# Kernel tuning notes

Measured on AMD Instinct MI355X. Metric: run time of the kernel, lower is better.

Reference implementation:

```python
import jax, jax.numpy as jnp
import numpy as np
from jax import lax

B, NPB = 4, 100000
N = B * NPB
C_BEV, C = 256, 64
H = W = 180
S = 10          # NUM_SWEEPS
MAXI = 64       # gt_boxes.shape[1] (max instances per sample)
NUMLOC = B * MAXI * S
NUMINST = B * MAXI
PC_MIN = -54.0
CELL = 0.075 * 8  # voxel * bev_image_stride


def setup_inputs() -> dict:
    key = jax.random.key(0)
    ks = jax.random.split(key, 20)
    pb = jnp.repeat(jnp.arange(B), NPB).astype(jnp.float32)
    xy = jax.random.uniform(ks[0], (N, 2), minval=-54.0, maxval=53.9)
    z = jax.random.uniform(ks[1], (N, 1), minval=-5.0, maxval=2.9)
    extra = jax.random.uniform(ks[2], (N, 2))
    sweep = jax.random.randint(ks[3], (N, 1), 0, S).astype(jnp.float32)
    inst = jax.random.randint(ks[4], (N, 1), 0, MAXI).astype(jnp.float32)
    points = jnp.concatenate([pb[:, None], xy, z, extra, sweep, inst, inst], axis=1)
    sc = 0.05
    return {
        'points': points,
        'spatial_features_2d': jax.random.normal(ks[5], (B, C_BEV, H, W)),
        'conv_w': jax.random.normal(ks[6], (C, C_BEV, 3, 3)) * sc,
        'bn_gamma': jnp.ones((C,)), 'bn_beta': jnp.zeros((C,)),
        'w_seg': jax.random.normal(ks[7], (C, 3)) * sc, 'b_seg': jnp.zeros((3,)),
        'w_reg': jax.random.normal(ks[8], (C, 3)) * sc, 'b_reg': jnp.zeros((3,)),
        'w_emb': jax.random.normal(ks[9], (C, 2)) * sc, 'b_emb': jnp.zeros((2,)),
        'w_shape': jax.random.normal(ks[10], (3, C)) * sc, 'b_shape': jnp.zeros((C,)),
        'w_tf': jax.random.normal(ks[11], (2 * C + 6, 7)) * sc, 'b_tf': jnp.zeros((7,)),
        'w_mos': jax.random.normal(ks[12], (C + 6, 1)) * sc, 'b_mos': jnp.zeros((1,)),
    }


def _forward(points, spatial_features_2d, conv_w, bn_gamma, bn_beta,
             w_seg, b_seg, w_reg, b_reg, w_emb, b_emb,
             w_shape, b_shape, w_tf, b_tf, w_mos, b_mos):
    # ---- shared_conv: Conv3x3 (no bias) + BatchNorm2d (training stats) + ReLU
    y = lax.conv_general_dilated(spatial_features_2d, conv_w, (1, 1), 'SAME',
                                 dimension_numbers=('NCHW', 'OIHW', 'NCHW'))
    mu = y.mean(axis=(0, 2, 3), keepdims=True)
    var = y.var(axis=(0, 2, 3), keepdims=True)
    y = (y - mu) * lax.rsqrt(var + 1e-5)
    bev = jax.nn.relu(y * bn_gamma[None, :, None, None] + bn_beta[None, :, None, None])
    bev_hwc = jnp.transpose(bev, (0, 2, 3, 1))  # [B,H,W,C]

    # ---- bilinear gather of BEV features at point locations (vectorized over batch)
    pb = points[:, 0].astype(jnp.int32)
    px = (points[:, 1] - PC_MIN) / CELL
    py = (points[:, 2] - PC_MIN) / CELL
    x0 = jnp.clip(jnp.floor(px).astype(jnp.int32), 0, W - 1)
    x1 = jnp.clip(x0 + 1, 0, W - 1)
    y0 = jnp.clip(jnp.floor(py).astype(jnp.int32), 0, H - 1)
    y1 = jnp.clip(y0 + 1, 0, H - 1)
    x0f, x1f = x0.astype(px.dtype), x1.astype(px.dtype)
    y0f, y1f = y0.astype(py.dtype), y1.astype(py.dtype)
    Ia = bev_hwc[pb, y0, x0]
    Ib = bev_hwc[pb, y1, x0]
    Ic = bev_hwc[pb, y0, x1]
    Id = bev_hwc[pb, y1, x1]
    wa = ((x1f - px) * (y1f - py))[:, None]
    wb = ((x1f - px) * (py - y0f))[:, None]
    wc = ((px - x0f) * (y1f - py))[:, None]
    wd = ((px - x0f) * (py - y0f))[:, None]
    points_feat = Ia * wa + Ib * wb + Ic * wc + Id * wd  # [N, C]

    # ---- point heads (single Linear each, mid_c=None)
    points_cls_logit = points_feat @ w_seg + b_seg
    points_offset = points_feat @ w_reg + b_reg
    points_embedding = points_feat @ w_emb + b_emb

    # ---- instance / local aggregation (training branch; all points foreground)
    sweep = points[:, 6].astype(jnp.int32)
    inst = points[:, 7].astype(jnp.int32)
    seg = (pb * MAXI + inst) * S + sweep  # dense local id in [0, NUMLOC)
    cnt = jax.ops.segment_sum(jnp.ones((N,), points.dtype), seg, NUMLOC)
    nonempty = cnt > 0
    xyz = points[:, 1:4]
    centroid = jax.ops.segment_sum(xyz, seg, NUMLOC) / jnp.clip(cnt, 1.0)[:, None]
    centered = xyz - centroid[seg]

    shape_enc = jax.ops.segment_max(centered @ w_shape + b_shape, seg, NUMLOC)
    shape_enc = jnp.where(nonempty[:, None], shape_enc, 0.0)
    locals_feat = jax.ops.segment_max(points_feat, seg, NUMLOC)
    locals_feat = jnp.where(nonempty[:, None], locals_feat, 0.0)
    locals_feat = locals_feat + shape_enc  # [NUMLOC, C]

    inst_of_local = jnp.arange(NUMLOC, dtype=jnp.int32) // S
    sweep_of_local = jnp.arange(NUMLOC, dtype=jnp.int32) % S
    neg_inf = jnp.array(-jnp.inf, locals_feat.dtype)
    globals_feat = jax.ops.segment_max(
        jnp.where(nonempty[:, None], locals_feat, neg_inf), inst_of_local, NUMINST)
    inst_nonempty = jax.ops.segment_max(nonempty, inst_of_local, NUMINST)
    globals_feat = jnp.where(inst_nonempty[:, None], globals_feat, 0.0)

    max_sweep = jax.ops.segment_max(jnp.where(nonempty, sweep_of_local, -1), inst_of_local, NUMINST)
    min_sweep = jax.ops.segment_min(jnp.where(nonempty, sweep_of_local, S), inst_of_local, NUMINST)
    inst_ids = jnp.arange(NUMINST, dtype=jnp.int32)
    idx_max = jnp.clip(inst_ids * S + max_sweep, 0, NUMLOC - 1)
    idx_min = jnp.clip(inst_ids * S + min_sweep, 0, NUMLOC - 1)
    init_center = centroid[idx_min]    # [NUMINST, 3]
    target_center = centroid[idx_max]  # [NUMINST, 3]

    locals_cat = jnp.concatenate(
        [locals_feat, globals_feat[inst_of_local], centroid, target_center[inst_of_local]], axis=1)
    locals_tf = locals_cat @ w_tf + b_tf  # [NUMLOC, 7]
    inst_feat = jnp.concatenate([globals_feat, init_center, target_center], axis=1)
    inst_mos = inst_feat @ w_mos + b_mos  # [NUMINST, 1]

    return points_cls_logit, points_offset, points_embedding, locals_tf, inst_mos


def reference(points, spatial_features_2d, conv_w, bn_gamma, bn_beta,
              w_seg, b_seg, w_reg, b_reg, w_emb, b_emb,
              w_shape, b_shape, w_tf, b_tf, w_mos, b_mos):
    return _forward(points, spatial_features_2d, conv_w, bn_gamma, bn_beta,
                    w_seg, b_seg, w_reg, b_reg, w_emb, b_emb,
                    w_shape, b_shape, w_tf, b_tf, w_mos, b_mos)
```

## Files before the change

### kernel.cpp

```cpp
#include <hip/hip_runtime.h>

typedef __attribute__((ext_vector_type(8))) unsigned short u16x8;
typedef __attribute__((ext_vector_type(8))) short s16x8;
typedef __attribute__((ext_vector_type(4))) float f32x4;

#define NPTS 400000
#define HW 32400
#define WID 180
#define NCI 256
#define NCO 64
#define NSEG 2560
#define NINST 256
#define NBLK 128
#define PPB 3125

__device__ __forceinline__ float bf2f(unsigned short u) {
  union { unsigned int i; float f; } v; v.i = ((unsigned int)u) << 16; return v.f;
}
__device__ __forceinline__ unsigned short f2bf(float f) {
  unsigned int u = __float_as_uint(f);
  return (unsigned short)((u + 0x7fffu + ((u >> 16) & 1u)) >> 16);
}

__device__ __forceinline__ void gld_lds16(const void* g, void* l) {
  __builtin_amdgcn_global_load_lds((const __attribute__((address_space(1))) void*)g,
                                   (__attribute__((address_space(3))) void*)l, 16, 0, 0);
}

__global__ __launch_bounds__(256) void k_transpose(const float* __restrict__ x,
                                                   unsigned short* __restrict__ xt) {
  const int bw = blockIdx.x;
  const int h = blockIdx.y, b = blockIdx.z;
  const int w0 = (bw >> 2) * 64, ci0 = (bw & 3) * 64;
  __shared__ float tile[64][68];
  const int t = threadIdx.x;
  const int a = t & 15, c4 = t >> 4;
  const int w4 = a * 4;
  const bool ldok = (w0 + w4) < WID;
#pragma unroll
  for (int it = 0; it < 4; ++it) {
    int ci = c4 + it * 16;
    float4 v = make_float4(0.f, 0.f, 0.f, 0.f);
    if (ldok) v = *(const float4*)(x + ((size_t)(b * NCI + ci0 + ci) * WID + h) * WID + w0 + w4);
    tile[w4 + 0][ci] = v.x;
    tile[w4 + 1][ci] = v.y;
    tile[w4 + 2][ci] = v.z;
    tile[w4 + 3][ci] = v.w;
  }
  __syncthreads();
  const int q = t & 7, r = t >> 3;
#pragma unroll
  for (int it = 0; it < 2; ++it) {
    int wl = r + it * 32;
    int w = w0 + wl;
    if (w >= WID) continue;
    const float* row = &tile[wl][q * 8];
    float4 lo = *(const float4*)(row);
    float4 hi = *(const float4*)(row + 4);
    u16x8 o;
    o[0] = f2bf(lo.x); o[1] = f2bf(lo.y); o[2] = f2bf(lo.z); o[3] = f2bf(lo.w);
    o[4] = f2bf(hi.x); o[5] = f2bf(hi.y); o[6] = f2bf(hi.z); o[7] = f2bf(hi.w);
    *(u16x8*)(xt + ((size_t)((b * WID + h) * WID + w)) * NCI + ci0 + q * 8) = o;
  }
}

__global__ void k_wreorg(const float* __restrict__ wt, unsigned short* __restrict__ wb) {
  int id = blockIdx.x * 256 + threadIdx.x;
  if (id >= 9 * 8 * 64 * 32) return;
  int cw = id & 31;
  int co = (id >> 5) & 63;
  int chunk = (id >> 11) & 7;
  int tap = id >> 14;
  int ci = chunk * 32 + cw;
  wb[id] = f2bf(wt[((size_t)co * 256 + ci) * 9 + tap]);
}

#define ROWB 6272
#define RBUF 25600
__global__ __launch_bounds__(256, 3) void k_conv_mfma(const unsigned short* __restrict__ xt,
                                                   const unsigned short* __restrict__ wb,
                                                   const float* __restrict__ zbuf,
                                                   unsigned short* __restrict__ y) {
  const int wg = blockIdx.x;
  const int lin = (wg & 7) * 90 + (wg >> 3);
  const int h2 = lin % 90;
  const int t2 = lin / 90;
  const int wth = t2 & 1, b = t2 >> 1;
  const int h0 = h2 * 2;
  const int w0 = wth * 96;
  __shared__ unsigned char strip[2][RBUF];
  const int tid = threadIdx.x;
  const int lane = tid & 63, wv = tid >> 6;
  const int mh = wv >> 1, nh = wv & 1;
  const int l15 = lane & 15, lk = lane >> 4;

  const char* srcs[7];
#pragma unroll
  for (int k = 0; k < 7; ++k) {
    int j = wv + k * 4;
    int g = j * 64 + lane;
    int pxlin = g >> 2, sub = g & 3;
    int row = pxlin / 98;
    int px = pxlin - row * 98;
    int hh = h0 + row - 1;
    int worig = w0 + px - 1;
    bool valid = (j < 25) && (pxlin < 392) &&
                 (hh >= 0) && (hh < WID) && (worig >= 0) && (worig < WID);
    int cig = sub ^ ((px >> 1) & 3);
    srcs[k] = valid
        ? (const char*)(xt + ((size_t)((b * WID + hh) * WID + worig)) * NCI + cig * 8)
        : (const char*)zbuf + lane * 16;
  }

  f32x4 acc[6][2];
#pragma unroll
  for (int i = 0; i < 6; ++i)
#pragma unroll
    for (int j = 0; j < 2; ++j) { acc[i][j][0] = 0.f; acc[i][j][1] = 0.f; acc[i][j][2] = 0.f; acc[i][j][3] = 0.f; }

  auto stage = [&](unsigned char* buf, int chunk) {
#pragma unroll
    for (int k = 0; k < 7; ++k) {
      int j = wv + k * 4;
      if (j >= 25) break;
      gld_lds16(srcs[k] + chunk * 64, buf + j * 1024);
    }
  };

  stage(strip[0], 0);
  asm volatile("s_waitcnt vmcnt(0)" ::: "memory");
  __syncthreads();

  const unsigned short* wco[2];
#pragma unroll
  for (int nf = 0; nf < 2; ++nf)
    wco[nf] = wb + (size_t)((nh * 2 + nf) * 16 + l15) * 32 + lk * 8;

  for (int chunk = 0; chunk < 8; ++chunk) {
    s16x8 bfr[9][2];
#pragma unroll
    for (int tap = 0; tap < 9; ++tap)
#pragma unroll
      for (int nf = 0; nf < 2; ++nf)
        bfr[tap][nf] = *(const s16x8*)(wco[nf] + (size_t)(tap * 8 + chunk) * 2048);
    if (chunk < 7) stage(strip[(chunk + 1) & 1], chunk + 1);
    const unsigned char* buf = strip[chunk & 1];
#pragma unroll
    for (int tap = 0; tap < 9; ++tap) {
      const int dh = tap / 3, dw = tap % 3;
      s16x8 afr[6];
#pragma unroll
      for (int i = 0; i < 6; ++i) {
        int wp = i * 16 + l15 + dw;
        int byte = (mh + dh) * ROWB + wp * 64 + ((lk ^ ((wp >> 1) & 3)) * 16);
        afr[i] = *(const s16x8*)(buf + byte);
      }
#pragma unroll
      for (int i = 0; i < 6; ++i)
#pragma unroll
        for (int nf = 0; nf < 2; ++nf)
          acc[i][nf] = __builtin_amdgcn_mfma_f32_16x16x32_bf16(afr[i], bfr[tap][nf], acc[i][nf], 0, 0, 0);
    }
    asm volatile("s_waitcnt vmcnt(0)" ::: "memory");
    __syncthreads();
  }

  const int r4 = lk * 4;
  const int hrow = h0 + mh;
#pragma unroll
  for (int i = 0; i < 6; ++i) {
#pragma unroll
    for (int nf = 0; nf < 2; ++nf) {
      int co = (nh * 2 + nf) * 16 + l15;
#pragma unroll
      for (int j = 0; j < 4; ++j) {
        int w = w0 + i * 16 + r4 + j;
        if (w < WID)
          y[((size_t)(b * HW) + hrow * WID + w) * 64 + co] = f2bf(acc[i][nf][j]);
      }
    }
  }
}

__global__ void k_stats2(const unsigned short* __restrict__ y, float* __restrict__ part) {
  const int t = threadIdx.x;
  const int c2 = (t & 31) * 2;
  const int g = t >> 5;
  float s0 = 0.f, s1 = 0.f, ss0 = 0.f, ss1 = 0.f;
  for (int r = blockIdx.x * 8 + g; r < 4 * HW; r += 256 * 8) {
    unsigned int v = *(const unsigned int*)(y + (size_t)r * 64 + c2);
    float f0 = bf2f((unsigned short)(v & 0xffffu));
    float f1 = bf2f((unsigned short)(v >> 16));
    s0 += f0; ss0 = fmaf(f0, f0, ss0);
    s1 += f1; ss1 = fmaf(f1, f1, ss1);
  }
  __shared__ float ls[8][64], lss[8][64];
  ls[g][c2] = s0; ls[g][c2 + 1] = s1;
  lss[g][c2] = ss0; lss[g][c2 + 1] = ss1;
  __syncthreads();
  if (t < 64) {
    float s = 0.f, ss = 0.f;
    for (int k = 0; k < 8; ++k) { s += ls[k][t]; ss += lss[k][t]; }
    part[(blockIdx.x * 64 + t) * 2] = s;
    part[(blockIdx.x * 64 + t) * 2 + 1] = ss;
  }
}

__global__ void k_bnparams(const float* __restrict__ part, const float* __restrict__ gamma,
                           const float* __restrict__ beta, float* __restrict__ ab) {
  const int t = threadIdx.x;
  float s = 0.f, ss = 0.f;
  for (int k = 0; k < 256; ++k) { s += part[(k * 64 + t) * 2]; ss += part[(k * 64 + t) * 2 + 1]; }
  float mu = s / 129600.f;
  float var = ss / 129600.f - mu * mu;
  float a = rsqrtf(var + 1e-5f) * gamma[t];
  ab[t * 2] = a; ab[t * 2 + 1] = beta[t] - mu * a;
}

__global__ void k_bn2(const unsigned short* __restrict__ y, const float* __restrict__ ab,
                      unsigned short* __restrict__ bev) {
  __shared__ float sa[64], sb[64];
  const int t = threadIdx.x;
  if (t < 64) { sa[t] = ab[t * 2]; sb[t] = ab[t * 2 + 1]; }
  __syncthreads();
  size_t id = (size_t)blockIdx.x * 256 + t;
  if (id >= (size_t)4 * HW * 8) return;
  int c0 = (int)(id & 7) * 8;
  u16x8 v = *(const u16x8*)(y + id * 8);
  u16x8 o;
#pragma unroll
  for (int k = 0; k < 8; ++k) {
    float f = fmaf(bf2f(v[k]), sa[c0 + k], sb[c0 + k]);
    o[k] = f2bf(f > 0.f ? f : 0.f);
  }
  *(u16x8*)(bev + id * 8) = o;
}

__global__ __launch_bounds__(256) void k_points(const float* __restrict__ pts,
                         const unsigned short* __restrict__ bev,
                         unsigned short* __restrict__ pf) {
  const int gid = blockIdx.x * 256 + threadIdx.x;
  const int lane = gid & 63;
  const int wid = gid >> 6;
#pragma unroll
  for (int it = 0; it < 4; ++it) {
    int p = wid * 4 + it;
    const float* pr = pts + (size_t)p * 9;
    float pbf = pr[0], xx = pr[1], yy = pr[2];
    int b = (int)pbf;
    float px = (xx - (-54.0f)) / 0.6f;
    float py = (yy - (-54.0f)) / 0.6f;
    int x0 = (int)floorf(px); x0 = min(max(x0, 0), WID - 1);
    int x1 = min(x0 + 1, WID - 1);
    int y0 = (int)floorf(py); y0 = min(max(y0, 0), WID - 1);
    int y1 = min(y0 + 1, WID - 1);
    float x0f = (float)x0, x1f = (float)x1, y0f = (float)y0, y1f = (float)y1;
    float wa = (x1f - px) * (y1f - py);
    float wb = (x1f - px) * (py - y0f);
    float wc = (px - x0f) * (y1f - py);
    float wd = (px - x0f) * (py - y0f);
    int i00 = y0 * WID + x0;
    int dx = x1 - x0;
    int dy = (y1 - y0) * WID;
    const unsigned short* bb = bev + ((size_t)b * HW) * 64 + lane;
    float Ia = bf2f(bb[(size_t)i00 * 64]);
    float Ic = bf2f(bb[(size_t)(i00 + dx) * 64]);
    float Ib = bf2f(bb[(size_t)(i00 + dy) * 64]);
    float Id = bf2f(bb[(size_t)(i00 + dy + dx) * 64]);
    float f = wa * Ia + wb * Ib + wc * Ic + wd * Id;
    pf[(size_t)p * 64 + lane] = f2bf(f);
  }
}

__global__ void k_heads(const unsigned short* __restrict__ pf,
                        const float* __restrict__ wseg, const float* __restrict__ bseg,
                        const float* __restrict__ wreg, const float* __restrict__ breg,
                        const float* __restrict__ wemb, const float* __restrict__ bemb,
                        float* __restrict__ ocls, float* __restrict__ ooff, float* __restrict__ oemb) {
  const int p = blockIdx.x * 256 + threadIdx.x;
  if (p >= NPTS) return;
  float a0 = bseg[0], a1 = bseg[1], a2 = bseg[2];
  float r0 = breg[0], r1 = breg[1], r2 = breg[2];
  float e0 = bemb[0], e1 = bemb[1];
  const u16x8* q = (const u16x8*)(pf + (size_t)p * 64);
#pragma unroll
  for (int g = 0; g < 8; ++g) {
    u16x8 v8 = q[g];
#pragma unroll
    for (int k = 0; k < 8; ++k) {
      int kk = g * 8 + k;
      float v = bf2f(v8[k]);
      a0 = fmaf(v, wseg[kk * 3 + 0], a0);
      a1 = fmaf(v, wseg[kk * 3 + 1], a1);
      a2 = fmaf(v, wseg[kk * 3 + 2], a2);
      r0 = fmaf(v, wreg[kk * 3 + 0], r0);
      r1 = fmaf(v, wreg[kk * 3 + 1], r1);
      r2 = fmaf(v, wreg[kk * 3 + 2], r2);
      e0 = fmaf(v, wemb[kk * 2 + 0], e0);
      e1 = fmaf(v, wemb[kk * 2 + 1], e1);
    }
  }
  ocls[p * 3 + 0] = a0; ocls[p * 3 + 1] = a1; ocls[p * 3 + 2] = a2;
  ooff[p * 3 + 0] = r0; ooff[p * 3 + 1] = r1; ooff[p * 3 + 2] = r2;
  oemb[p * 2 + 0] = e0; oemb[p * 2 + 1] = e1;
}

__global__ __launch_bounds__(256) void k_hist2(const float* __restrict__ pts,
                                               int* __restrict__ seg, int* __restrict__ rankp,
                                               int* __restrict__ bh) {
  __shared__ int lc[NSEG];
  const int t = threadIdx.x, blk = blockIdx.x;
  for (int i = t; i < NSEG; i += 256) lc[i] = 0;
  __syncthreads();
  const int p0 = blk * PPB;
  for (int i = t; i < PPB; i += 256) {
    int p = p0 + i;
    const float* pr = pts + (size_t)p * 9;
    int b = (int)pr[0];
    int sw = (int)pr[6];
    int ins = (int)pr[7];
    int s = (b * 64 + ins) * 10 + sw;
    seg[p] = s;
    rankp[p] = atomicAdd(&lc[s], 1);
  }
  __syncthreads();
  for (int i = t; i < NSEG; i += 256) bh[i * NBLK + blk] = lc[i];
}

__global__ void k_scan2a(const int* __restrict__ bh, int* __restrict__ basebk,
                         int* __restrict__ tot) {
  const int s = blockIdx.x * 256 + threadIdx.x;
  int acc = 0;
  for (int b = 0; b < NBLK; ++b) {
    int v = bh[s * NBLK + b];
    basebk[s * NBLK + b] = acc;
    acc += v;
  }
  tot[s] = acc;
}

__global__ void k_scan2b(const int* __restrict__ tot, int* __restrict__ base,
                         int* __restrict__ cnt) {
  __shared__ int csum[256];
  const int t = threadIdx.x;
  int loc[10]; int run = 0;
#pragma unroll
  for (int k = 0; k < 10; ++k) { loc[k] = tot[t * 10 + k]; run += loc[k]; }
  csum[t] = run;
  __syncthreads();
  if (t == 0) {
    int a = 0;
    for (int i = 0; i < 256; ++i) { int v = csum[i]; csum[i] = a; a += v; }
  }
  __syncthreads();
  int acc = csum[t];
#pragma unroll
  for (int k = 0; k < 10; ++k) {
    int s = t * 10 + k;
    base[s] = acc; cnt[s] = loc[k];
    acc += loc[k];
  }
}

__global__ void k_scatter2(const int* __restrict__ seg, const int* __restrict__ rankp,
                           const int* __restrict__ base, const int* __restrict__ basebk,
                           int* __restrict__ order) {
  const int p = blockIdx.x * 256 + threadIdx.x;
  if (p < NPTS) {
    int s = seg[p];
    int blk = p / PPB;
    order[base[s] + basebk[s * NBLK + blk] + rankp[p]] = p;
  }
}

__global__ __launch_bounds__(256) void k_seg(const int* __restrict__ cnt, const int* __restrict__ base,
                      const int* __restrict__ order, const float* __restrict__ pts,
                      const unsigned short* __restrict__ pf,
                      const float* __restrict__ wsh, const float* __restrict__ bsh,
                      float* __restrict__ lf, float* __restrict__ centroid,
                      int* __restrict__ nonempty) {
  const int s = blockIdx.x;
  const int t = threadIdx.x, lane = t & 63, wv = t >> 6;
  const int n = cnt[s], bs = base[s];
  float sx = 0.f, sy = 0.f, sz = 0.f;
  for (int i = t; i < n; i += 256) {
    int p = order[bs + i];
    const float* pr = pts + (size_t)p * 9;
    sx += pr[1]; sy += pr[2]; sz += pr[3];
  }
#pragma unroll
  for (int m = 32; m > 0; m >>= 1) {
    sx += __shfl_xor(sx, m); sy += __shfl_xor(sy, m); sz += __shfl_xor(sz, m);
  }
  __shared__ float red[3][4];
  __shared__ float csh[3];
  if (lane == 0) { red[0][wv] = sx; red[1][wv] = sy; red[2][wv] = sz; }
  __syncthreads();
  if (t == 0) {
    float dn = (float)max(n, 1);
    csh[0] = (red[0][0] + red[0][1] + red[0][2] + red[0][3]) / dn;
    csh[1] = (red[1][0] + red[1][1] + red[1][2] + red[1][3]) / dn;
    csh[2] = (red[2][0] + red[2][1] + red[2][2] + red[2][3]) / dn;
  }
  __syncthreads();
  const float cx = csh[0], cy = csh[1], cz = csh[2];
  const float w0 = wsh[lane], w1 = wsh[64 + lane], w2 = wsh[128 + lane], bb = bsh[lane];
  float smax = -INFINITY, lmax = -INFINITY;
  for (int i = wv; i < n; i += 4) {
    int p = order[bs + i];
    const float* pr = pts + (size_t)p * 9;
    float sv = fmaf(pr[1] - cx, w0, fmaf(pr[2] - cy, w1, fmaf(pr[3] - cz, w2, bb)));
    smax = fmaxf(smax, sv);
    lmax = fmaxf(lmax, bf2f(pf[(size_t)p * 64 + lane]));
  }
  __shared__ float rs[4][64], rl[4][64];
  rs[wv][lane] = smax; rl[wv][lane] = lmax;
  __syncthreads();
  if (wv == 0) {
    smax = fmaxf(fmaxf(rs[0][lane], rs[1][lane]), fmaxf(rs[2][lane], rs[3][lane]));
    lmax = fmaxf(fmaxf(rl[0][lane], rl[1][lane]), fmaxf(rl[2][lane], rl[3][lane]));
    bool ne = n > 0;
    lf[s * 64 + lane] = (ne ? lmax : 0.f) + (ne ? smax : 0.f);
    if (lane == 0) {
      nonempty[s] = ne ? 1 : 0;
      centroid[s * 3 + 0] = cx; centroid[s * 3 + 1] = cy; centroid[s * 3 + 2] = cz;
    }
  }
}

__global__ void k_glob(const float* __restrict__ lf, const int* __restrict__ ne,
                       const float* __restrict__ centroid,
                       const float* __restrict__ wmos, const float* __restrict__ bmos,
                       float* __restrict__ gf, float* __restrict__ tc, float* __restrict__ ic,
                       float* __restrict__ omos) {
  const int i = blockIdx.x;
  const int t = threadIdx.x;
  float g = -INFINITY;
  int maxsw = -1, minsw = 10;
  bool any = false;
#pragma unroll
  for (int s = 0; s < 10; ++s) {
    int idx = i * 10 + s;
    bool e = ne[idx] != 0;
    float v = lf[idx * 64 + t];
    g = fmaxf(g, e ? v : -INFINITY);
    if (e) { any = true; maxsw = s; minsw = min(minsw, s); }
  }
  float gv = any ? g : 0.f;
  gf[i * 64 + t] = gv;
  int idxmax = min(max(i * 10 + maxsw, 0), NSEG - 1);
  int idxmin = min(max(i * 10 + minsw, 0), NSEG - 1);
  float tcx = centroid[idxmax * 3 + 0], tcy = centroid[idxmax * 3 + 1], tcz = centroid[idxmax * 3 + 2];
  float icx = centroid[idxmin * 3 + 0], icy = centroid[idxmin * 3 + 1], icz = centroid[idxmin * 3 + 2];
  if (t == 0) {
    tc[i * 3 + 0] = tcx; tc[i * 3 + 1] = tcy; tc[i * 3 + 2] = tcz;
    ic[i * 3 + 0] = icx; ic[i * 3 + 1] = icy; ic[i * 3 + 2] = icz;
  }
  float r = gv * wmos[t];
#pragma unroll
  for (int m = 32; m > 0; m >>= 1) r += __shfl_xor(r, m);
  if (t == 0) {
    r += icx * wmos[64] + icy * wmos[65] + icz * wmos[66];
    r += tcx * wmos[67] + tcy * wmos[68] + tcz * wmos[69];
    omos[i] = r + bmos[0];
  }
}

__global__ void k_tf(const float* __restrict__ lf, const float* __restrict__ gf,
                     const float* __restrict__ centroid, const float* __restrict__ tc,
                     const float* __restrict__ wtf, const float* __restrict__ btf,
                     float* __restrict__ otf) {
  const int r = blockIdx.x * 256 + threadIdx.x;
  if (r >= NSEG) return;
  const int i = r / 10;
  float acc[7];
#pragma unroll
  for (int j = 0; j < 7; ++j) acc[j] = btf[j];
  for (int k = 0; k < 64; ++k) {
    float v = lf[r * 64 + k];
#pragma unroll
    for (int j = 0; j < 7; ++j) acc[j] = fmaf(v, wtf[k * 7 + j], acc[j]);
  }
  for (int k = 0; k < 64; ++k) {
    float v = gf[i * 64 + k];
#pragma unroll
    for (int j = 0; j < 7; ++j) acc[j] = fmaf(v, wtf[(64 + k) * 7 + j], acc[j]);
  }
#pragma unroll
  for (int c = 0; c < 3; ++c) {
    float v = centroid[r * 3 + c];
#pragma unroll
    for (int j = 0; j < 7; ++j) acc[j] = fmaf(v, wtf[(128 + c) * 7 + j], acc[j]);
  }
#pragma unroll
  for (int c = 0; c < 3; ++c) {
    float v = tc[i * 3 + c];
#pragma unroll
    for (int j = 0; j < 7; ++j) acc[j] = fmaf(v, wtf[(131 + c) * 7 + j], acc[j]);
  }
#pragma unroll
  for (int j = 0; j < 7; ++j) otf[r * 7 + j] = acc[j];
}

extern "C" void kernel_launch(void* const* d_in, const int* in_sizes, int n_in,
                              void* d_out, int out_size, void* d_ws, size_t ws_size,
                              hipStream_t stream) {
  const float* pts   = (const float*)d_in[0];
  const float* x     = (const float*)d_in[1];
  const float* convw = (const float*)d_in[2];
  const float* gamma = (const float*)d_in[3];
  const float* beta  = (const float*)d_in[4];
  const float* wseg  = (const float*)d_in[5];
  const float* bseg  = (const float*)d_in[6];
  const float* wreg  = (const float*)d_in[7];
  const float* breg  = (const float*)d_in[8];
  const float* wemb  = (const float*)d_in[9];
  const float* bemb  = (const float*)d_in[10];
  const float* wsh   = (const float*)d_in[11];
  const float* bsh   = (const float*)d_in[12];
  const float* wtf   = (const float*)d_in[13];
  const float* btf   = (const float*)d_in[14];
  const float* wmos  = (const float*)d_in[15];
  const float* bmos  = (const float*)d_in[16];

  float* out = (float*)d_out;
  float* o_cls = out;
  float* o_off = out + 1200000;
  float* o_emb = out + 2400000;
  float* o_tf  = out + 3200000;
  float* o_mos = out + 3217920;

  char* wsp = (char*)d_ws;
  size_t off = 0;
  auto alloc = [&](size_t bytes) -> void* {
    void* p = wsp + off;
    off = (off + bytes + 255) & ~(size_t)255;
    return p;
  };
  unsigned short* xt   = (unsigned short*)alloc((size_t)4 * WID * WID * NCI * 2);
  unsigned short* pf   = xt;
  unsigned short* wbuf = (unsigned short*)alloc((size_t)9 * 8 * 64 * 32 * 2);
  unsigned short* y    = (unsigned short*)alloc((size_t)4 * HW * 64 * 2);
  unsigned short* bev  = (unsigned short*)alloc((size_t)4 * HW * 64 * 2);
  int*   seg      = (int*)alloc((size_t)NPTS * 4);
  int*   rankp    = (int*)alloc((size_t)NPTS * 4);
  int*   order    = (int*)alloc((size_t)NPTS * 4);
  int*   bh       = (int*)alloc((size_t)NSEG * NBLK * 4);
  int*   basebk   = (int*)alloc((size_t)NSEG * NBLK * 4);
  int*   tot      = (int*)alloc(NSEG * 4);
  int*   cnt      = (int*)alloc(NSEG * 4);
  int*   base     = (int*)alloc(NSEG * 4);
  float* part     = (float*)alloc(256 * 64 * 2 * 4);
  float* ab       = (float*)alloc(64 * 2 * 4);
  float* centroid = (float*)alloc(NSEG * 3 * 4);
  float* lf       = (float*)alloc(NSEG * 64 * 4);
  int*   nonem    = (int*)alloc(NSEG * 4);
  float* gf       = (float*)alloc(NINST * 64 * 4);
  float* tc       = (float*)alloc(NINST * 3 * 4);
  float* ic       = (float*)alloc(NINST * 3 * 4);
  float* zbuf     = (float*)alloc(2048);
  (void)ws_size; (void)n_in; (void)in_sizes; (void)out_size;

  hipMemsetAsync(zbuf, 0, 2048, stream);

  k_hist2<<<NBLK, 256, 0, stream>>>(pts, seg, rankp, bh);
  k_scan2a<<<10, 256, 0, stream>>>(bh, basebk, tot);
  k_scan2b<<<1, 256, 0, stream>>>(tot, base, cnt);
  k_scatter2<<<(NPTS + 255) / 256, 256, 0, stream>>>(seg, rankp, base, basebk, order);
  k_transpose<<<dim3(12, WID, 4), 256, 0, stream>>>(x, xt);
  k_wreorg<<<576, 256, 0, stream>>>(convw, wbuf);
  k_conv_mfma<<<720, 256, 0, stream>>>(xt, wbuf, zbuf, y);
  k_stats2<<<256, 256, 0, stream>>>(y, part);
  k_bnparams<<<1, 64, 0, stream>>>(part, gamma, beta, ab);
  k_bn2<<<(4 * HW * 8 + 255) / 256, 256, 0, stream>>>(y, ab, bev);
  k_points<<<25000, 256, 0, stream>>>(pts, bev, pf);
  k_heads<<<(NPTS + 255) / 256, 256, 0, stream>>>(pf, wseg, bseg, wreg, breg, wemb, bemb,
                                                  o_cls, o_off, o_emb);
  k_seg<<<NSEG, 256, 0, stream>>>(cnt, base, order, pts, pf, wsh, bsh, lf, centroid, nonem);
  k_glob<<<NINST, 64, 0, stream>>>(lf, nonem, centroid, wmos, bmos, gf, tc, ic, o_mos);
  k_tf<<<(NSEG + 255) / 256, 256, 0, stream>>>(lf, gf, centroid, tc, wtf, btf, o_tf);
}
```

Before: 308.4 us.

## Fuse BN statistics into conv epilogue and BN-apply into point sampling

The conv kernel now accumulates per-channel sum and sum-of-squares from its fp32 accumulators and writes per-workgroup partials, so the separate stats pass over y is gone. The BN+ReLU pass that wrote a bev tensor is also removed. The affine transform and ReLU are applied on the fly to the four bilinear taps inside k_points. Separately, the histogram block count is raised and the per-segment scan is vectorised with int4. The cost is extra epilogue work and an LDS reduction in the conv, a longer serial reduction in bnparams (720 partials), and recomputing BN per sampled tap. Statistics now come from fp32 values rather than bf16-rounded ones.

```diff
diff --git a/kernel.cpp b/kernel.cpp
--- a/kernel.cpp
+++ b/kernel.cpp
@@ -11,8 +11,8 @@
 #define NCO 64
 #define NSEG 2560
 #define NINST 256
-#define NBLK 128
-#define PPB 3125
+#define NBLK 500
+#define PPB 800
 
 __device__ __forceinline__ float bf2f(unsigned short u) {
   union { unsigned int i; float f; } v; v.i = ((unsigned int)u) << 16; return v.f;
@@ -80,7 +80,8 @@
 __global__ __launch_bounds__(256, 3) void k_conv_mfma(const unsigned short* __restrict__ xt,
                                                    const unsigned short* __restrict__ wb,
                                                    const float* __restrict__ zbuf,
-                                                   unsigned short* __restrict__ y) {
+                                                   unsigned short* __restrict__ y,
+                                                   float* __restrict__ part) {
   const int wg = blockIdx.x;
   const int lin = (wg & 7) * 90 + (wg >> 3);
   const int h2 = lin % 90;
@@ -89,6 +90,7 @@
   const int h0 = h2 * 2;
   const int w0 = wth * 96;
   __shared__ unsigned char strip[2][RBUF];
+  __shared__ float redS[2][2][2][16], redQ[2][2][2][16];
   const int tid = threadIdx.x;
   const int lane = tid & 63, wv = tid >> 6;
   const int mh = wv >> 1, nh = wv & 1;
@@ -167,6 +169,7 @@
 
   const int r4 = lk * 4;
   const int hrow = h0 + mh;
+  float s[2] = {0.f, 0.f}, q[2] = {0.f, 0.f};
 #pragma unroll
   for (int i = 0; i < 6; ++i) {
 #pragma unroll
@@ -175,34 +178,29 @@
 #pragma unroll
       for (int j = 0; j < 4; ++j) {
         int w = w0 + i * 16 + r4 + j;
-        if (w < WID)
-          y[((size_t)(b * HW) + hrow * WID + w) * 64 + co] = f2bf(acc[i][nf][j]);
+        if (w < WID) {
+          float v = acc[i][nf][j];
+          y[((size_t)(b * HW) + hrow * WID + w) * 64 + co] = f2bf(v);
+          s[nf] += v; q[nf] = fmaf(v, v, q[nf]);
+        }
       }
     }
   }
-}
-
-__global__ void k_stats2(const unsigned short* __restrict__ y, float* __restrict__ part) {
-  const int t = threadIdx.x;
-  const int c2 = (t & 31) * 2;
-  const int g = t >> 5;
-  float s0 = 0.f, s1 = 0.f, ss0 = 0.f, ss1 = 0.f;
-  for (int r = blockIdx.x * 8 + g; r < 4 * HW; r += 256 * 8) {
-    unsigned int v = *(const unsigned int*)(y + (size_t)r * 64 + c2);
-    float f0 = bf2f((unsigned short)(v & 0xffffu));
-    float f1 = bf2f((unsigned short)(v >> 16));
-    s0 += f0; ss0 = fmaf(f0, f0, ss0);
-    s1 += f1; ss1 = fmaf(f1, f1, ss1);
-  }
-  __shared__ float ls[8][64], lss[8][64];
-  ls[g][c2] = s0; ls[g][c2 + 1] = s1;
-  lss[g][c2] = ss0; lss[g][c2 + 1] = ss1;
-  __syncthreads();
-  if (t < 64) {
-    float s = 0.f, ss = 0.f;
-    for (int k = 0; k < 8; ++k) { s += ls[k][t]; ss += lss[k][t]; }
-    part[(blockIdx.x * 64 + t) * 2] = s;
-    part[(blockIdx.x * 64 + t) * 2 + 1] = ss;
+#pragma unroll
+  for (int nf = 0; nf < 2; ++nf) {
+    s[nf] += __shfl_xor(s[nf], 16); s[nf] += __shfl_xor(s[nf], 32);
+    q[nf] += __shfl_xor(q[nf], 16); q[nf] += __shfl_xor(q[nf], 32);
+  }
+  if (lk == 0) {
+#pragma unroll
+    for (int nf = 0; nf < 2; ++nf) { redS[mh][nh][nf][l15] = s[nf]; redQ[mh][nh][nf][l15] = q[nf]; }
+  }
+  __syncthreads();
+  if (tid < 64) {
+    int co = tid;
+    int nhh = co >> 5, nff = (co >> 4) & 1, ll = co & 15;
+    part[((size_t)wg * 64 + co) * 2 + 0] = redS[0][nhh][nff][ll] + redS[1][nhh][nff][ll];
+    part[((size_t)wg * 64 + co) * 2 + 1] = redQ[0][nhh][nff][ll] + redQ[1][nhh][nff][ll];
   }
 }
 
@@ -210,38 +208,21 @@
                            const float* __restrict__ beta, float* __restrict__ ab) {
   const int t = threadIdx.x;
   float s = 0.f, ss = 0.f;
-  for (int k = 0; k < 256; ++k) { s += part[(k * 64 + t) * 2]; ss += part[(k * 64 + t) * 2 + 1]; }
+  for (int k = 0; k < 720; ++k) { s += part[((size_t)k * 64 + t) * 2]; ss += part[((size_t)k * 64 + t) * 2 + 1]; }
   float mu = s / 129600.f;
   float var = ss / 129600.f - mu * mu;
   float a = rsqrtf(var + 1e-5f) * gamma[t];
   ab[t * 2] = a; ab[t * 2 + 1] = beta[t] - mu * a;
 }
 
-__global__ void k_bn2(const unsigned short* __restrict__ y, const float* __restrict__ ab,
-                      unsigned short* __restrict__ bev) {
-  __shared__ float sa[64], sb[64];
-  const int t = threadIdx.x;
-  if (t < 64) { sa[t] = ab[t * 2]; sb[t] = ab[t * 2 + 1]; }
-  __syncthreads();
-  size_t id = (size_t)blockIdx.x * 256 + t;
-  if (id >= (size_t)4 * HW * 8) return;
-  int c0 = (int)(id & 7) * 8;
-  u16x8 v = *(const u16x8*)(y + id * 8);
-  u16x8 o;
-#pragma unroll
-  for (int k = 0; k < 8; ++k) {
-    float f = fmaf(bf2f(v[k]), sa[c0 + k], sb[c0 + k]);
-    o[k] = f2bf(f > 0.f ? f : 0.f);
-  }
-  *(u16x8*)(bev + id * 8) = o;
-}
-
 __global__ __launch_bounds__(256) void k_points(const float* __restrict__ pts,
-                         const unsigned short* __restrict__ bev,
+                         const unsigned short* __restrict__ y,
+                         const float* __restrict__ ab,
                          unsigned short* __restrict__ pf) {
   const int gid = blockIdx.x * 256 + threadIdx.x;
   const int lane = gid & 63;
   const int wid = gid >> 6;
+  const float sa = ab[lane * 2], sb = ab[lane * 2 + 1];
 #pragma unroll
   for (int it = 0; it < 4; ++it) {
     int p = wid * 4 + it;
@@ -262,11 +243,11 @@
     int i00 = y0 * WID + x0;
     int dx = x1 - x0;
     int dy = (y1 - y0) * WID;
-    const unsigned short* bb = bev + ((size_t)b * HW) * 64 + lane;
-    float Ia = bf2f(bb[(size_t)i00 * 64]);
-    float Ic = bf2f(bb[(size_t)(i00 + dx) * 64]);
-    float Ib = bf2f(bb[(size_t)(i00 + dy) * 64]);
-    float Id = bf2f(bb[(size_t)(i00 + dy + dx) * 64]);
+    const unsigned short* bb = y + ((size_t)b * HW) * 64 + lane;
+    float Ia = fmaf(bf2f(bb[(size_t)i00 * 64]), sa, sb);            Ia = Ia > 0.f ? Ia : 0.f;
+    float Ic = fmaf(bf2f(bb[(size_t)(i00 + dx) * 64]), sa, sb);     Ic = Ic > 0.f ? Ic : 0.f;
+    float Ib = fmaf(bf2f(bb[(size_t)(i00 + dy) * 64]), sa, sb);     Ib = Ib > 0.f ? Ib : 0.f;
+    float Id = fmaf(bf2f(bb[(size_t)(i00 + dy + dx) * 64]), sa, sb); Id = Id > 0.f ? Id : 0.f;
     float f = wa * Ia + wb * Ib + wc * Ic + wd * Id;
     pf[(size_t)p * 64 + lane] = f2bf(f);
   }
@@ -330,11 +311,17 @@
 __global__ void k_scan2a(const int* __restrict__ bh, int* __restrict__ basebk,
                          int* __restrict__ tot) {
   const int s = blockIdx.x * 256 + threadIdx.x;
+  const int4* row = (const int4*)(bh + (size_t)s * NBLK);
+  int4* brow = (int4*)(basebk + (size_t)s * NBLK);
   int acc = 0;
-  for (int b = 0; b < NBLK; ++b) {
-    int v = bh[s * NBLK + b];
-    basebk[s * NBLK + b] = acc;
-    acc += v;
+  for (int b = 0; b < NBLK / 4; ++b) {
+    int4 v = row[b];
+    int4 o;
+    o.x = acc; acc += v.x;
+    o.y = acc; acc += v.y;
+    o.z = acc; acc += v.z;
+    o.w = acc; acc += v.w;
+    brow[b] = o;
   }
   tot[s] = acc;
 }
@@ -541,7 +528,6 @@
   unsigned short* pf   = xt;
   unsigned short* wbuf = (unsigned short*)alloc((size_t)9 * 8 * 64 * 32 * 2);
   unsigned short* y    = (unsigned short*)alloc((size_t)4 * HW * 64 * 2);
-  unsigned short* bev  = (unsigned short*)alloc((size_t)4 * HW * 64 * 2);
   int*   seg      = (int*)alloc((size_t)NPTS * 4);
   int*   rankp    = (int*)alloc((size_t)NPTS * 4);
   int*   order    = (int*)alloc((size_t)NPTS * 4);
@@ -550,7 +536,7 @@
   int*   tot      = (int*)alloc(NSEG * 4);
   int*   cnt      = (int*)alloc(NSEG * 4);
   int*   base     = (int*)alloc(NSEG * 4);
-  float* part     = (float*)alloc(256 * 64 * 2 * 4);
+  float* part     = (float*)alloc((size_t)720 * 64 * 2 * 4);
   float* ab       = (float*)alloc(64 * 2 * 4);
   float* centroid = (float*)alloc(NSEG * 3 * 4);
   float* lf       = (float*)alloc(NSEG * 64 * 4);
@@ -569,11 +555,9 @@
   k_scatter2<<<(NPTS + 255) / 256, 256, 0, stream>>>(seg, rankp, base, basebk, order);
   k_transpose<<<dim3(12, WID, 4), 256, 0, stream>>>(x, xt);
   k_wreorg<<<576, 256, 0, stream>>>(convw, wbuf);
-  k_conv_mfma<<<720, 256, 0, stream>>>(xt, wbuf, zbuf, y);
-  k_stats2<<<256, 256, 0, stream>>>(y, part);
+  k_conv_mfma<<<720, 256, 0, stream>>>(xt, wbuf, zbuf, y, part);
   k_bnparams<<<1, 64, 0, stream>>>(part, gamma, beta, ab);
-  k_bn2<<<(4 * HW * 8 + 255) / 256, 256, 0, stream>>>(y, ab, bev);
-  k_points<<<25000, 256, 0, stream>>>(pts, bev, pf);
+  k_points<<<25000, 256, 0, stream>>>(pts, y, ab, pf);
   k_heads<<<(NPTS + 255) / 256, 256, 0, stream>>>(pf, wseg, bseg, wreg, breg, wemb, bemb,
                                                   o_cls, o_off, o_emb);
   k_seg<<<NSEG, 256, 0, stream>>>(cnt, base, order, pts, pf, wsh, bsh, lf, centroid, nonem);
```

Result: slower. 327.8 us (+6.3%).
